# Performance work log

Measured on AMD Instinct MI355X. Metric: run time of the kernel, lower is better.

## Reference

```python
import jax, jax.numpy as jnp
import numpy as np

N_NODES = 50000
N_EDGES = 600000
DIM = 128
N_HEADS = 3
EDGE_VOCAB = 22754
NEG_SLOPE = 0.2


def setup_inputs() -> dict:
    key = jax.random.key(0)
    ks = jax.random.split(key, 12)
    s = 1.0 / np.sqrt(DIM)
    return {
        "x": jax.random.normal(ks[0], (N_NODES, DIM), dtype=jnp.float32),
        "edge_index": jax.random.randint(ks[1], (2, N_EDGES), 0, N_NODES, dtype=jnp.int64),
        "edge_ids": jax.random.randint(ks[2], (N_EDGES,), 0, EDGE_VOCAB, dtype=jnp.int64),
        "ddi_weight": jax.random.uniform(ks[3], (N_EDGES,), dtype=jnp.float32),
        "W_lin": jax.random.normal(ks[4], (DIM, DIM), dtype=jnp.float32) * s,
        "b_lin": jnp.zeros((DIM,), dtype=jnp.float32),
        "edge_emb": jax.random.normal(ks[5], (EDGE_VOCAB, 1), dtype=jnp.float32) * 0.1,
        "W_heads": jax.random.normal(ks[6], (N_HEADS, DIM, DIM), dtype=jnp.float32) * s,
        "att_src": jax.random.normal(ks[7], (N_HEADS, DIM), dtype=jnp.float32) * s,
        "att_dst": jax.random.normal(ks[8], (N_HEADS, DIM), dtype=jnp.float32) * s,
        "bias_heads": jnp.zeros((N_HEADS, DIM), dtype=jnp.float32),
    }


def _gat_head(x, src, dst, ew, W, a_src, a_dst, bias):
    # x: [N, D] (already passed through shared lin), ew: [E] scalar edge weights
    h = x @ W                                   # [N, D]
    e = jax.nn.leaky_relu(
        (h @ a_src)[src] + (h @ a_dst)[dst], NEG_SLOPE)   # [E]
    # segment softmax over destination nodes
    e_max = jax.ops.segment_max(e, dst, num_segments=N_NODES)   # [N]
    e_exp = jnp.exp(e - e_max[dst])                              # [E]
    denom = jax.ops.segment_sum(e_exp, dst, num_segments=N_NODES)
    alpha = e_exp / jnp.maximum(denom[dst], 1e-16)               # [E]
    msg = (alpha * ew)[:, None] * h[src]                         # [E, D]
    return jax.ops.segment_sum(msg, dst, num_segments=N_NODES) + bias


def reference(x, edge_index, edge_ids, ddi_weight, W_lin, b_lin, edge_emb,
              W_heads, att_src, att_dst, bias_heads):
    x = x @ W_lin + b_lin                         # shared linear projection
    ew = edge_emb[edge_ids, 0] - ddi_weight        # [E]
    src, dst = edge_index[0], edge_index[1]
    out = jnp.zeros_like(x)
    for hix in range(N_HEADS):                     # small fixed head count
        out = out + _gat_head(x, src, dst, ew, W_heads[hix],
                              att_src[hix], att_dst[hix], bias_heads[hix])
    return out / N_HEADS
```

## Files before the change

kernel.cpp:

```cpp
#include <hip/hip_runtime.h>
#include <math.h>

#define NN 50000
#define NE 600000
#define D 128
#define NH 3
#define CAP 64
#define CSTRIDE 16
#define EDGE_BLOCKS ((NE + 255) / 256)
#define MFMA_BLOCKS ((NN + 63) / 64)
#define LOG2E 1.44269504088896340736f

typedef short bf16x8 __attribute__((ext_vector_type(8)));
typedef _Float16 f16x8 __attribute__((ext_vector_type(8)));
typedef float f32x4 __attribute__((ext_vector_type(4)));

extern "C" __device__ float __ocml_native_exp2_f32(float);

__device__ __forceinline__ unsigned short f2b(float f) {
  unsigned int u = __float_as_uint(f);
  u += 0x7FFF + ((u >> 16) & 1);
  return (unsigned short)(u >> 16);
}
__device__ __forceinline__ float blo(unsigned int u) {
  return __uint_as_float(u << 16);
}
__device__ __forceinline__ float bhi(unsigned int u) {
  return __uint_as_float(u & 0xffff0000u);
}
__device__ __forceinline__ unsigned short f2h(float f) {
  _Float16 t = (_Float16)f;
  return *(unsigned short*)&t;
}

__global__ __launch_bounds__(256) void pack_scatter2(const float* __restrict__ W_lin,
                                                     const float* __restrict__ W_heads,
                                                     const float* __restrict__ att_src,
                                                     const float* __restrict__ att_dst,
                                                     const float* __restrict__ b_lin,
                                                     const float* __restrict__ bias_heads,
                                                     const int* __restrict__ ei,
                                                     const int* __restrict__ eid,
                                                     const float* __restrict__ ddi,
                                                     const float* __restrict__ emb,
                                                     uint4* __restrict__ Bpack,
                                                     uint4* __restrict__ Wpack3,
                                                     float* __restrict__ sbuf,
                                                     float* __restrict__ bcomb2,
                                                     int* __restrict__ counts,
                                                     unsigned int* __restrict__ slots8) {
  const int bx = blockIdx.x;
  const int tid = threadIdx.x;
  if (bx < EDGE_BLOCKS) {
    int e = bx * 256 + tid;
    if (e < NE) {
      int src = ei[e], dst = ei[NE + e];
      int idx = atomicAdd(&counts[dst * CSTRIDE], 1);
      idx = idx < CAP ? idx : CAP - 1;
      float ew = emb[eid[e]] - ddi[e];
      slots8[dst * CAP + idx] = (unsigned int)src | ((unsigned int)f2b(ew) << 16);
    }
    return;
  }
  const int pb = bx - EDGE_BLOCKS;
  if (pb < 8) {
    int r = pb * 256 + tid;
    int nt = r >> 8, s = (r >> 6) & 3, q = (r >> 4) & 3, n0 = r & 15;
    int kbase = s * 32 + q * 8;
    int n = nt * 16 + n0;
    unsigned int w[4];
    #pragma unroll
    for (int p = 0; p < 4; ++p) {
      unsigned short lo = f2b(W_lin[(kbase + 2 * p) * D + n]);
      unsigned short hi = f2b(W_lin[(kbase + 2 * p + 1) * D + n]);
      w[p] = (unsigned int)lo | ((unsigned int)hi << 16);
    }
    Bpack[r] = make_uint4(w[0], w[1], w[2], w[3]);
  } else if (pb < 32) {
    int u = (pb - 8) * 256 + tid;
    int h = u >> 11, r = u & 2047;
    int nt = r >> 8, s = (r >> 6) & 3, q = (r >> 4) & 3, n0 = r & 15;
    int kbase = s * 32 + q * 8;
    int n = nt * 16 + n0;
    const float* W = W_heads + (size_t)h * D * D;
    unsigned int w[4];
    #pragma unroll
    for (int p = 0; p < 4; ++p) {
      unsigned short lo = f2h(W[(kbase + 2 * p) * D + n]);
      unsigned short hi = f2h(W[(kbase + 2 * p + 1) * D + n]);
      w[p] = (unsigned int)lo | ((unsigned int)hi << 16);
    }
    Wpack3[h * 2048 + r] = make_uint4(w[0], w[1], w[2], w[3]);
  } else if (pb < 35) {
    const int h = pb - 32;
    __shared__ float wha_s[128], wha_d[128], scs[128], scd[128];
    {
      int m = tid & 127;
      const float* W = W_heads + (size_t)h * D * D + m * D;
      const float* a = (tid < 128) ? (att_src + h * D) : (att_dst + h * D);
      float acc = 0.f;
      for (int n = 0; n < D; ++n) acc += W[n] * a[n];
      if (tid < 128) wha_s[m] = acc; else wha_d[m] = acc;
    }
    __syncthreads();
    {
      int k = tid & 127;
      const float* wl = W_lin + k * D;
      const float* wha = (tid < 128) ? wha_s : wha_d;
      float acc = 0.f;
      for (int m = 0; m < D; ++m) acc += wl[m] * wha[m];
      if (tid < 128) scs[k] = acc * LOG2E; else scd[k] = acc * LOG2E;
    }
    __syncthreads();
    if (tid < 2) {
      const float* wha = tid ? wha_d : wha_s;
      float a = 0.f;
      for (int k = 0; k < D; ++k) a += b_lin[k] * wha[k];
      sbuf[h * 2 + tid] = a * LOG2E;
    }
    {
      int s = (tid >> 6) & 3, q = (tid >> 4) & 3, n0 = tid & 15;
      int kbase = s * 32 + q * 8;
      bool mine = (n0 < 6) && ((n0 >> 1) == h);
      bool zero = (h == 0) && (n0 >= 6);
      if (mine || zero) {
        float vals[8];
        #pragma unroll
        for (int j = 0; j < 8; ++j)
          vals[j] = zero ? 0.f : ((n0 & 1) ? scd[kbase + j] : scs[kbase + j]);
        unsigned int w[4];
        #pragma unroll
        for (int p = 0; p < 4; ++p)
          w[p] = (unsigned int)f2b(vals[2 * p]) | ((unsigned int)f2b(vals[2 * p + 1]) << 16);
        Bpack[2048 + tid] = make_uint4(w[0], w[1], w[2], w[3]);
      }
    }
  } else {
    if (tid < D)
      bcomb2[tid] = (bias_heads[tid] + bias_heads[D + tid] + bias_heads[2 * D + tid]) * (1.f / 3.f);
  }
}

__global__ __launch_bounds__(256) void mfma_x(const float* __restrict__ x,
                                              const uint4* __restrict__ Bpack,
                                              const float* __restrict__ b_lin,
                                              const float* __restrict__ sbuf,
                                              unsigned short* __restrict__ xb,
                                              float* __restrict__ s_src4,
                                              float* __restrict__ s_dst4) {
  const int row0 = blockIdx.x * 64;
  const int tid = threadIdx.x;
  __shared__ __align__(16) unsigned short As[64][136];
  #pragma unroll
  for (int it = 0; it < 8; ++it) {
    int idx = tid + it * 256;
    int m = idx >> 5, k4 = idx & 31;
    int row = row0 + m;
    float4 v = make_float4(0.f, 0.f, 0.f, 0.f);
    if (row < NN) v = ((const float4*)(x + (size_t)row * D))[k4];
    uint2 pk;
    pk.x = (unsigned int)f2b(v.x) | ((unsigned int)f2b(v.y) << 16);
    pk.y = (unsigned int)f2b(v.z) | ((unsigned int)f2b(v.w) << 16);
    *((uint2*)&As[m][k4 * 4]) = pk;
  }
  __syncthreads();
  const int wv = tid >> 6;
  const int lane = tid & 63;
  const int n0 = lane & 15, q = lane >> 4;
  const int boff = q * 16 + n0;
  const bf16x8* Bp = (const bf16x8*)Bpack;

  bf16x8 a4[4];
  #pragma unroll
  for (int s = 0; s < 4; ++s)
    a4[s] = *(const bf16x8*)&As[wv * 16 + n0][s * 32 + q * 8];

  f32x4 acc[9];
  #pragma unroll
  for (int nt = 0; nt < 9; ++nt) acc[nt] = (f32x4){0.f, 0.f, 0.f, 0.f};

  #pragma unroll
  for (int s = 0; s < 4; ++s) {
    #pragma unroll
    for (int nt = 0; nt < 9; ++nt) {
      bf16x8 b = Bp[(nt * 4 + s) * 64 + boff];
      acc[nt] = __builtin_amdgcn_mfma_f32_16x16x32_bf16(a4[s], b, acc[nt], 0, 0, 0);
    }
  }
  __syncthreads();
  #pragma unroll
  for (int nt = 0; nt < 8; ++nt) {
    int col = nt * 16 + n0;
    float bv = b_lin[col];
    #pragma unroll
    for (int r = 0; r < 4; ++r)
      As[wv * 16 + q * 4 + r][col] = f2b(acc[nt][r] + bv);
  }
  if (n0 < 6) {
    float sb = sbuf[n0];
    float* Sout = (n0 & 1) ? s_dst4 : s_src4;
    #pragma unroll
    for (int r = 0; r < 4; ++r) {
      int row = row0 + wv * 16 + q * 4 + r;
      if (row < NN) Sout[row * 4 + (n0 >> 1)] = acc[8][r] + sb;
    }
  }
  __syncthreads();
  #pragma unroll
  for (int i = 0; i < 4; ++i) {
    int idx = tid + i * 256;
    int row = idx >> 4, c16 = idx & 15;
    int grow = row0 + row;
    if (grow < NN)
      *((uint4*)&xb[(size_t)grow * D + c16 * 8]) = *((const uint4*)&As[row][c16 * 8]);
  }
}

__global__ __launch_bounds__(64) void gather12n(const int* __restrict__ counts,
                                                const unsigned int* __restrict__ slots8,
                                                const float4* __restrict__ s_src4,
                                                const float4* __restrict__ s_dst4,
                                                const unsigned short* __restrict__ xb,
                                                unsigned short* __restrict__ accb) {
  const int dst = blockIdx.x;
  const int lane = threadIdx.x;
  const int hf = lane >> 5;
  const int c = (lane & 31) * 4;
  int cnt = counts[dst * CSTRIDE];
  cnt = cnt < CAP ? cnt : CAP;
  const int beg = dst * CAP;
  const int end = beg + cnt;
  float4 sd = s_dst4[dst];
  float a0[4] = {0.f, 0.f, 0.f, 0.f};
  float a1[4] = {0.f, 0.f, 0.f, 0.f};
  float a2[4] = {0.f, 0.f, 0.f, 0.f};
  float d0 = 0.f, d1 = 0.f, d2 = 0.f;
  int s = beg + hf;
  for (; s + 2 < end; s += 4) {
    unsigned int seA = slots8[s];
    unsigned int seB = slots8[s + 2];
    int srcA = seA & 0xffffu, srcB = seB & 0xffffu;
    float ewA = bhi(seA), ewB = bhi(seB);
    float4 ssA = s_src4[srcA];
    float4 ssB = s_src4[srcB];
    uint2 ua = *(const uint2*)&xb[(size_t)srcA * D + c];
    uint2 ub = *(const uint2*)&xb[(size_t)srcB * D + c];
    float vA0 = ssA.x + sd.x, vA1 = ssA.y + sd.y, vA2 = ssA.z + sd.z;
    float vB0 = ssB.x + sd.x, vB1 = ssB.y + sd.y, vB2 = ssB.z + sd.z;
    vA0 = fmaxf(vA0, 0.2f * vA0);
    vA1 = fmaxf(vA1, 0.2f * vA1);
    vA2 = fmaxf(vA2, 0.2f * vA2);
    vB0 = fmaxf(vB0, 0.2f * vB0);
    vB1 = fmaxf(vB1, 0.2f * vB1);
    vB2 = fmaxf(vB2, 0.2f * vB2);
    float pA0 = __ocml_native_exp2_f32(vA0);
    float pA1 = __ocml_native_exp2_f32(vA1);
    float pA2 = __ocml_native_exp2_f32(vA2);
    float pB0 = __ocml_native_exp2_f32(vB0);
    float pB1 = __ocml_native_exp2_f32(vB1);
    float pB2 = __ocml_native_exp2_f32(vB2);
    float wa0 = pA0 * ewA, wa1 = pA1 * ewA, wa2 = pA2 * ewA;
    float wb0 = pB0 * ewB, wb1 = pB1 * ewB, wb2 = pB2 * ewB;
    float xA[4] = {blo(ua.x), bhi(ua.x), blo(ua.y), bhi(ua.y)};
    float xB[4] = {blo(ub.x), bhi(ub.x), blo(ub.y), bhi(ub.y)};
    #pragma unroll
    for (int j = 0; j < 4; ++j) {
      a0[j] += wa0 * xA[j] + wb0 * xB[j];
      a1[j] += wa1 * xA[j] + wb1 * xB[j];
      a2[j] += wa2 * xA[j] + wb2 * xB[j];
    }
    d0 += pA0 + pB0;
    d1 += pA1 + pB1;
    d2 += pA2 + pB2;
  }
  if (s < end) {
    unsigned int seA = slots8[s];
    int srcA = seA & 0xffffu;
    float ewA = bhi(seA);
    float4 ssA = s_src4[srcA];
    uint2 ua = *(const uint2*)&xb[(size_t)srcA * D + c];
    float vA0 = ssA.x + sd.x, vA1 = ssA.y + sd.y, vA2 = ssA.z + sd.z;
    vA0 = fmaxf(vA0, 0.2f * vA0);
    vA1 = fmaxf(vA1, 0.2f * vA1);
    vA2 = fmaxf(vA2, 0.2f * vA2);
    float pA0 = __ocml_native_exp2_f32(vA0);
    float pA1 = __ocml_native_exp2_f32(vA1);
    float pA2 = __ocml_native_exp2_f32(vA2);
    float w0 = pA0 * ewA, w1 = pA1 * ewA, w2 = pA2 * ewA;
    float xA[4] = {blo(ua.x), bhi(ua.x), blo(ua.y), bhi(ua.y)};
    #pragma unroll
    for (int j = 0; j < 4; ++j) {
      a0[j] += w0 * xA[j];
      a1[j] += w1 * xA[j];
      a2[j] += w2 * xA[j];
    }
    d0 += pA0; d1 += pA1; d2 += pA2;
  }
  #pragma unroll
  for (int j = 0; j < 4; ++j) {
    a0[j] += __shfl_xor(a0[j], 32, 64);
    a1[j] += __shfl_xor(a1[j], 32, 64);
    a2[j] += __shfl_xor(a2[j], 32, 64);
  }
  d0 += __shfl_xor(d0, 32, 64);
  d1 += __shfl_xor(d1, 32, 64);
  d2 += __shfl_xor(d2, 32, 64);
  if (hf == 0) {
    float r0 = 1.f / (3.f * fmaxf(d0, 1e-16f));
    float r1 = 1.f / (3.f * fmaxf(d1, 1e-16f));
    float r2 = 1.f / (3.f * fmaxf(d2, 1e-16f));
    unsigned short* base = accb + (size_t)dst * (NH * D);
    uint2 o;
    o.x = (unsigned int)f2h(a0[0] * r0) | ((unsigned int)f2h(a0[1] * r0) << 16);
    o.y = (unsigned int)f2h(a0[2] * r0) | ((unsigned int)f2h(a0[3] * r0) << 16);
    *(uint2*)&base[c] = o;
    o.x = (unsigned int)f2h(a1[0] * r1) | ((unsigned int)f2h(a1[1] * r1) << 16);
    o.y = (unsigned int)f2h(a1[2] * r1) | ((unsigned int)f2h(a1[3] * r1) << 16);
    *(uint2*)&base[D + c] = o;
    o.x = (unsigned int)f2h(a2[0] * r2) | ((unsigned int)f2h(a2[1] * r2) << 16);
    o.y = (unsigned int)f2h(a2[2] * r2) | ((unsigned int)f2h(a2[3] * r2) << 16);
    *(uint2*)&base[2 * D + c] = o;
  }
}

__global__ __launch_bounds__(256) void final_gemm16(const unsigned short* __restrict__ accb,
                                                    const uint4* __restrict__ Wpack3,
                                                    const float* __restrict__ bcomb2,
                                                    float* __restrict__ out) {
  const int row0 = blockIdx.x * 64;
  const int tid = threadIdx.x;
  __shared__ __align__(16) _Float16 Af[64][136];
  const int wv = tid >> 6;
  const int lane = tid & 63;
  const int n0 = lane & 15, q = lane >> 4;
  const int boff = q * 16 + n0;

  f32x4 o[8];
  #pragma unroll
  for (int nt = 0; nt < 8; ++nt) o[nt] = (f32x4){0.f, 0.f, 0.f, 0.f};

  for (int ck = 0; ck < NH; ++ck) {
    if (ck) __syncthreads();
    #pragma unroll
    for (int it = 0; it < 4; ++it) {
      int idx = tid + it * 256;
      int m = idx >> 4, k8 = idx & 15;
      int row = row0 + m;
      uint4 u = make_uint4(0, 0, 0, 0);
      if (row < NN)
        u = *(const uint4*)&accb[(size_t)row * (NH * D) + ck * D + k8 * 8];
      *((uint4*)&Af[m][k8 * 8]) = u;
    }
    __syncthreads();
    f16x8 af[4];
    #pragma unroll
    for (int s = 0; s < 4; ++s)
      af[s] = *(const f16x8*)&Af[wv * 16 + n0][s * 32 + q * 8];
    const f16x8* Bp = (const f16x8*)(Wpack3 + ck * 2048);
    #pragma unroll
    for (int s = 0; s < 4; ++s) {
      #pragma unroll
      for (int nt = 0; nt < 8; ++nt) {
        f16x8 b = Bp[(nt * 4 + s) * 64 + boff];
        o[nt] = __builtin_amdgcn_mfma_f32_16x16x32_f16(af[s], b, o[nt], 0, 0, 0);
      }
    }
  }
  #pragma unroll
  for (int nt = 0; nt < 8; ++nt) {
    int col = nt * 16 + n0;
    float bv = bcomb2[col];
    #pragma unroll
    for (int r = 0; r < 4; ++r) {
      int row = row0 + wv * 16 + q * 4 + r;
      if (row < NN) out[(size_t)row * D + col] = o[nt][r] + bv;
    }
  }
}

extern "C" void kernel_launch(void* const* d_in, const int* in_sizes, int n_in,
                              void* d_out, int out_size, void* d_ws, size_t ws_size,
                              hipStream_t stream) {
  const float* x          = (const float*)d_in[0];
  const int*   ei         = (const int*)d_in[1];
  const int*   eid        = (const int*)d_in[2];
  const float* ddi        = (const float*)d_in[3];
  const float* W_lin      = (const float*)d_in[4];
  const float* b_lin      = (const float*)d_in[5];
  const float* emb        = (const float*)d_in[6];
  const float* W_heads    = (const float*)d_in[7];
  const float* att_src    = (const float*)d_in[8];
  const float* att_dst    = (const float*)d_in[9];
  const float* bias_heads = (const float*)d_in[10];
  float* out = (float*)d_out;

  uint4*  Bpack  = (uint4*)d_ws;
  uint4*  Wpack3 = Bpack + 2304;
  unsigned short* xb = (unsigned short*)(Wpack3 + NH * 2048);
  unsigned int* slots8 = (unsigned int*)(xb + (size_t)NN * D);
  unsigned short* accb = (unsigned short*)(slots8 + (size_t)NN * CAP);
  float*  sbuf   = (float*)(accb + (size_t)NN * NH * D);
  float*  bcomb2 = sbuf + 8;
  float*  s_src4 = bcomb2 + 128;
  float*  s_dst4 = s_src4 + (size_t)NN * 4;
  int*    counts = (int*)(s_dst4 + (size_t)NN * 4);

  hipMemsetAsync(counts, 0, (size_t)NN * CSTRIDE * sizeof(int), stream);
  pack_scatter2<<<EDGE_BLOCKS + 36, 256, 0, stream>>>(
      W_lin, W_heads, att_src, att_dst, b_lin, bias_heads, ei, eid, ddi, emb,
      Bpack, Wpack3, sbuf, bcomb2, counts, slots8);
  mfma_x<<<MFMA_BLOCKS, 256, 0, stream>>>(x, Bpack, b_lin, sbuf, xb,
                                          s_src4, s_dst4);
  gather12n<<<NN, 64, 0, stream>>>(counts, slots8, (const float4*)s_src4,
                                   (const float4*)s_dst4, xb, accb);
  final_gemm16<<<MFMA_BLOCKS, 256, 0, stream>>>(accb, Wpack3, bcomb2, out);
}
```

Baseline: 207.3 us.

## Restructure gather to score one edge per lane and broadcast weights via shuffles

The per-destination gather kernel is reorganized. Each lane now computes the attention logits, exponentials and softmax denominators for one incoming edge, with the denominators reduced by a butterfly shuffle. The aggregation loop then walks the edges sequentially: it broadcasts each edge's source index and weights with shuffles, and each lane accumulates two feature columns, reading from a 4-deep prefetch buffer of row loads. This removes the redundant per-lane exp and leaky-relu work of the previous split-half design. In exchange the loop is serialized over all edges with shuffles per step, and the dynamically indexed prefetch array risks being placed in scratch memory.

After: 226.9 us. +9.5%, slower.

```diff
diff --git a/kernel.cpp b/kernel.cpp
--- a/kernel.cpp
+++ b/kernel.cpp
@@ -216,111 +216,76 @@
   }
 }
 
-__global__ __launch_bounds__(64) void gather12n(const int* __restrict__ counts,
-                                                const unsigned int* __restrict__ slots8,
-                                                const float4* __restrict__ s_src4,
-                                                const float4* __restrict__ s_dst4,
-                                                const unsigned short* __restrict__ xb,
-                                                unsigned short* __restrict__ accb) {
+__global__ __launch_bounds__(64) void gather13(const int* __restrict__ counts,
+                                               const unsigned int* __restrict__ slots8,
+                                               const float4* __restrict__ s_src4,
+                                               const float4* __restrict__ s_dst4,
+                                               const unsigned short* __restrict__ xb,
+                                               unsigned short* __restrict__ accb) {
   const int dst = blockIdx.x;
   const int lane = threadIdx.x;
-  const int hf = lane >> 5;
-  const int c = (lane & 31) * 4;
   int cnt = counts[dst * CSTRIDE];
   cnt = cnt < CAP ? cnt : CAP;
-  const int beg = dst * CAP;
-  const int end = beg + cnt;
+  const bool valid = lane < cnt;
   float4 sd = s_dst4[dst];
-  float a0[4] = {0.f, 0.f, 0.f, 0.f};
-  float a1[4] = {0.f, 0.f, 0.f, 0.f};
-  float a2[4] = {0.f, 0.f, 0.f, 0.f};
-  float d0 = 0.f, d1 = 0.f, d2 = 0.f;
-  int s = beg + hf;
-  for (; s + 2 < end; s += 4) {
-    unsigned int seA = slots8[s];
-    unsigned int seB = slots8[s + 2];
-    int srcA = seA & 0xffffu, srcB = seB & 0xffffu;
-    float ewA = bhi(seA), ewB = bhi(seB);
-    float4 ssA = s_src4[srcA];
-    float4 ssB = s_src4[srcB];
-    uint2 ua = *(const uint2*)&xb[(size_t)srcA * D + c];
-    uint2 ub = *(const uint2*)&xb[(size_t)srcB * D + c];
-    float vA0 = ssA.x + sd.x, vA1 = ssA.y + sd.y, vA2 = ssA.z + sd.z;
-    float vB0 = ssB.x + sd.x, vB1 = ssB.y + sd.y, vB2 = ssB.z + sd.z;
-    vA0 = fmaxf(vA0, 0.2f * vA0);
-    vA1 = fmaxf(vA1, 0.2f * vA1);
-    vA2 = fmaxf(vA2, 0.2f * vA2);
-    vB0 = fmaxf(vB0, 0.2f * vB0);
-    vB1 = fmaxf(vB1, 0.2f * vB1);
-    vB2 = fmaxf(vB2, 0.2f * vB2);
-    float pA0 = __ocml_native_exp2_f32(vA0);
-    float pA1 = __ocml_native_exp2_f32(vA1);
-    float pA2 = __ocml_native_exp2_f32(vA2);
-    float pB0 = __ocml_native_exp2_f32(vB0);
-    float pB1 = __ocml_native_exp2_f32(vB1);
-    float pB2 = __ocml_native_exp2_f32(vB2);
-    float wa0 = pA0 * ewA, wa1 = pA1 * ewA, wa2 = pA2 * ewA;
-    float wb0 = pB0 * ewB, wb1 = pB1 * ewB, wb2 = pB2 * ewB;
-    float xA[4] = {blo(ua.x), bhi(ua.x), blo(ua.y), bhi(ua.y)};
-    float xB[4] = {blo(ub.x), bhi(ub.x), blo(ub.y), bhi(ub.y)};
-    #pragma unroll
-    for (int j = 0; j < 4; ++j) {
-      a0[j] += wa0 * xA[j] + wb0 * xB[j];
-      a1[j] += wa1 * xA[j] + wb1 * xB[j];
-      a2[j] += wa2 * xA[j] + wb2 * xB[j];
-    }
-    d0 += pA0 + pB0;
-    d1 += pA1 + pB1;
-    d2 += pA2 + pB2;
-  }
-  if (s < end) {
-    unsigned int seA = slots8[s];
-    int srcA = seA & 0xffffu;
-    float ewA = bhi(seA);
-    float4 ssA = s_src4[srcA];
-    uint2 ua = *(const uint2*)&xb[(size_t)srcA * D + c];
-    float vA0 = ssA.x + sd.x, vA1 = ssA.y + sd.y, vA2 = ssA.z + sd.z;
-    vA0 = fmaxf(vA0, 0.2f * vA0);
-    vA1 = fmaxf(vA1, 0.2f * vA1);
-    vA2 = fmaxf(vA2, 0.2f * vA2);
-    float pA0 = __ocml_native_exp2_f32(vA0);
-    float pA1 = __ocml_native_exp2_f32(vA1);
-    float pA2 = __ocml_native_exp2_f32(vA2);
-    float w0 = pA0 * ewA, w1 = pA1 * ewA, w2 = pA2 * ewA;
-    float xA[4] = {blo(ua.x), bhi(ua.x), blo(ua.y), bhi(ua.y)};
-    #pragma unroll
-    for (int j = 0; j < 4; ++j) {
-      a0[j] += w0 * xA[j];
-      a1[j] += w1 * xA[j];
-      a2[j] += w2 * xA[j];
-    }
-    d0 += pA0; d1 += pA1; d2 += pA2;
-  }
-  #pragma unroll
-  for (int j = 0; j < 4; ++j) {
-    a0[j] += __shfl_xor(a0[j], 32, 64);
-    a1[j] += __shfl_xor(a1[j], 32, 64);
-    a2[j] += __shfl_xor(a2[j], 32, 64);
-  }
-  d0 += __shfl_xor(d0, 32, 64);
-  d1 += __shfl_xor(d1, 32, 64);
-  d2 += __shfl_xor(d2, 32, 64);
-  if (hf == 0) {
-    float r0 = 1.f / (3.f * fmaxf(d0, 1e-16f));
-    float r1 = 1.f / (3.f * fmaxf(d1, 1e-16f));
-    float r2 = 1.f / (3.f * fmaxf(d2, 1e-16f));
-    unsigned short* base = accb + (size_t)dst * (NH * D);
-    uint2 o;
-    o.x = (unsigned int)f2h(a0[0] * r0) | ((unsigned int)f2h(a0[1] * r0) << 16);
-    o.y = (unsigned int)f2h(a0[2] * r0) | ((unsigned int)f2h(a0[3] * r0) << 16);
-    *(uint2*)&base[c] = o;
-    o.x = (unsigned int)f2h(a1[0] * r1) | ((unsigned int)f2h(a1[1] * r1) << 16);
-    o.y = (unsigned int)f2h(a1[2] * r1) | ((unsigned int)f2h(a1[3] * r1) << 16);
-    *(uint2*)&base[D + c] = o;
-    o.x = (unsigned int)f2h(a2[0] * r2) | ((unsigned int)f2h(a2[1] * r2) << 16);
-    o.y = (unsigned int)f2h(a2[2] * r2) | ((unsigned int)f2h(a2[3] * r2) << 16);
-    *(uint2*)&base[2 * D + c] = o;
-  }
+
+  unsigned int se = slots8[dst * CAP + lane];
+  int src = valid ? (int)(se & 0xffffu) : 0;
+  float ew = bhi(se);
+  float4 ss = s_src4[src];
+  float v0 = ss.x + sd.x, v1 = ss.y + sd.y, v2 = ss.z + sd.z;
+  v0 = fmaxf(v0, 0.2f * v0);
+  v1 = fmaxf(v1, 0.2f * v1);
+  v2 = fmaxf(v2, 0.2f * v2);
+  float p0 = __ocml_native_exp2_f32(v0);
+  float p1 = __ocml_native_exp2_f32(v1);
+  float p2 = __ocml_native_exp2_f32(v2);
+  p0 = valid ? p0 : 0.f;
+  p1 = valid ? p1 : 0.f;
+  p2 = valid ? p2 : 0.f;
+  float w0 = p0 * ew, w1 = p1 * ew, w2 = p2 * ew;
+
+  float d0 = p0, d1 = p1, d2 = p2;
+  #pragma unroll
+  for (int off = 1; off < 64; off <<= 1) {
+    d0 += __shfl_xor(d0, off, 64);
+    d1 += __shfl_xor(d1, off, 64);
+    d2 += __shfl_xor(d2, off, 64);
+  }
+
+  float a00 = 0.f, a01 = 0.f, a10 = 0.f, a11 = 0.f, a20 = 0.f, a21 = 0.f;
+  unsigned int ubuf[4];
+  const int npre = cnt < 4 ? cnt : 4;
+  for (int kp = 0; kp < npre; ++kp) {
+    int sk = __shfl(src, kp, 64);
+    ubuf[kp] = *(const unsigned int*)&xb[(size_t)sk * D + lane * 2];
+  }
+  for (int k = 0; k < cnt; ++k) {
+    unsigned int u = ubuf[k & 3];
+    int kn = k + 4;
+    if (kn < cnt) {
+      int sk = __shfl(src, kn, 64);
+      ubuf[kn & 3] = *(const unsigned int*)&xb[(size_t)sk * D + lane * 2];
+    }
+    float w0k = __shfl(w0, k, 64);
+    float w1k = __shfl(w1, k, 64);
+    float w2k = __shfl(w2, k, 64);
+    float xl = blo(u), xh = bhi(u);
+    a00 += w0k * xl; a01 += w0k * xh;
+    a10 += w1k * xl; a11 += w1k * xh;
+    a20 += w2k * xl; a21 += w2k * xh;
+  }
+
+  float r0 = 1.f / (3.f * fmaxf(d0, 1e-16f));
+  float r1 = 1.f / (3.f * fmaxf(d1, 1e-16f));
+  float r2 = 1.f / (3.f * fmaxf(d2, 1e-16f));
+  unsigned short* base = accb + (size_t)dst * (NH * D);
+  *(unsigned int*)&base[2 * lane] =
+      (unsigned int)f2h(a00 * r0) | ((unsigned int)f2h(a01 * r0) << 16);
+  *(unsigned int*)&base[D + 2 * lane] =
+      (unsigned int)f2h(a10 * r1) | ((unsigned int)f2h(a11 * r1) << 16);
+  *(unsigned int*)&base[2 * D + 2 * lane] =
+      (unsigned int)f2h(a20 * r2) | ((unsigned int)f2h(a21 * r2) << 16);
 }
 
 __global__ __launch_bounds__(256) void final_gemm16(const unsigned short* __restrict__ accb,
@@ -411,7 +376,7 @@
       Bpack, Wpack3, sbuf, bcomb2, counts, slots8);
   mfma_x<<<MFMA_BLOCKS, 256, 0, stream>>>(x, Bpack, b_lin, sbuf, xb,
                                           s_src4, s_dst4);
-  gather12n<<<NN, 64, 0, stream>>>(counts, slots8, (const float4*)s_src4,
-                                   (const float4*)s_dst4, xb, accb);
+  gather13<<<NN, 64, 0, stream>>>(counts, slots8, (const float4*)s_src4,
+                                  (const float4*)s_dst4, xb, accb);
   final_gemm16<<<MFMA_BLOCKS, 256, 0, stream>>>(accb, Wpack3, bcomb2, out);
 }
```
